# Kernel optimization log

Hardware: AMD Instinct MI355X
Metric: run time of the kernel (lower is better)

## Reference

```python
import jax, jax.numpy as jnp
import numpy as np

N_NODES = 100000
N_EDGES = 1600000
IN_DIM = 128
HID = 128
HEADS = 4
HEAD_DIM = HID // HEADS
OUT_DIM = 3
N_GRAPHS = 1024
BN_EPS = 1e-5


def setup_inputs() -> dict:
    key = jax.random.key(0)
    ks = jax.random.split(key, 32)
    inp = {}
    inp['x'] = jax.random.normal(ks[0], (N_NODES, IN_DIM), dtype=jnp.float32)
    inp['edge_index'] = jax.random.randint(ks[1], (2, N_EDGES), 0, N_NODES, dtype=jnp.int64)
    inp['edge_attr'] = jax.random.normal(ks[2], (N_EDGES,), dtype=jnp.float32)
    inp['batch'] = jnp.sort(jax.random.randint(ks[3], (N_NODES,), 0, N_GRAPHS, dtype=jnp.int64))
    s = 0.05
    inp['gat_w'] = jax.random.normal(ks[4], (IN_DIM, HID), jnp.float32) * s
    inp['gat_att_src'] = jax.random.normal(ks[5], (HEADS, HEAD_DIM), jnp.float32) * s
    inp['gat_att_dst'] = jax.random.normal(ks[6], (HEADS, HEAD_DIM), jnp.float32) * s
    inp['gat_b'] = jnp.zeros((HID,), jnp.float32)
    for i, k in zip((1, 2, 3), (ks[7], ks[8], ks[9])):
        inp[f'gcn{i}_w'] = jax.random.normal(k, (HID, HID), jnp.float32) * s
        inp[f'gcn{i}_b'] = jnp.zeros((HID,), jnp.float32)
        inp[f'bn{i}_g'] = jnp.ones((HID,), jnp.float32)
        inp[f'bn{i}_b'] = jnp.zeros((HID,), jnp.float32)
        inp[f'bn{i}_m'] = jax.random.normal(jax.random.fold_in(key, 100 + i), (HID,), jnp.float32) * 0.01
        inp[f'bn{i}_v'] = jnp.ones((HID,), jnp.float32)
    inp['p1_w'] = jax.random.normal(ks[10], (HID, HID), jnp.float32) * s
    inp['p1_b'] = jnp.zeros((HID,), jnp.float32)
    inp['p2_w'] = jax.random.normal(ks[11], (HID, HID // 2), jnp.float32) * s
    inp['p2_b'] = jnp.zeros((HID // 2,), jnp.float32)
    inp['cls_w'] = jax.random.normal(ks[12], (HID // 2, OUT_DIM), jnp.float32) * s
    inp['cls_b'] = jnp.zeros((OUT_DIM,), jnp.float32)
    return inp


def _add_self_loops(edge_index, n):
    ar = jnp.arange(n, dtype=edge_index.dtype)
    return jnp.concatenate([edge_index, jnp.stack([ar, ar])], axis=1)


def _gat(x, ei, w, att_src, att_dst, bias):
    # PyG GATConv: per-head linear, additive attention, softmax over incoming edges.
    n = x.shape[0]
    h = (x @ w).reshape(n, HEADS, HEAD_DIM)
    a_src = jnp.einsum('nhd,hd->nh', h, att_src)  # [N,H]
    a_dst = jnp.einsum('nhd,hd->nh', h, att_dst)
    src, dst = ei[0], ei[1]
    e = jax.nn.leaky_relu(a_src[src] + a_dst[dst], 0.2)  # [E,H]
    m = jax.ops.segment_max(e, dst, num_segments=n)       # per-dst max
    e = jnp.exp(e - m[dst])
    denom = jax.ops.segment_sum(e, dst, num_segments=n)
    alpha = e / denom[dst]                                 # self-loops => denom > 0
    msg = h[src] * alpha[:, :, None]                       # [E,H,D]
    out = jax.ops.segment_sum(msg, dst, num_segments=n)
    return out.reshape(n, HID) + bias


def _gcn(x, ei, w, bias):
    # PyG GCNConv with symmetric normalization and self-loops (already added).
    n = x.shape[0]
    src, dst = ei[0], ei[1]
    deg = jax.ops.segment_sum(jnp.ones_like(dst, dtype=x.dtype), dst, num_segments=n)
    dinv = jnp.where(deg > 0, jax.lax.rsqrt(deg), 0.0)
    norm = dinv[src] * dinv[dst]                           # [E]
    xw = x @ w
    out = jax.ops.segment_sum(norm[:, None] * xw[src], dst, num_segments=n)
    return out + bias


def _bn(x, g, b, m, v):
    return (x - m) * jax.lax.rsqrt(v + BN_EPS) * g + b


def reference(x, edge_index, edge_attr, batch,
              gat_w, gat_att_src, gat_att_dst, gat_b,
              gcn1_w, gcn1_b, gcn2_w, gcn2_b, gcn3_w, gcn3_b,
              bn1_g, bn1_b, bn1_m, bn1_v,
              bn2_g, bn2_b, bn2_m, bn2_v,
              bn3_g, bn3_b, bn3_m, bn3_v,
              p1_w, p1_b, p2_w, p2_b, cls_w, cls_b):
    n = x.shape[0]
    ei = _add_self_loops(edge_index, n)
    # eval mode: dropout is identity, BN uses running stats
    h = jax.nn.elu(_gat(x, ei, gat_w, gat_att_src, gat_att_dst, gat_b))
    idn = h
    h = jax.nn.elu(_bn(_gcn(h, ei, gcn1_w, gcn1_b), bn1_g, bn1_b, bn1_m, bn1_v)) + idn
    idn = h
    h = jax.nn.elu(_bn(_gcn(h, ei, gcn2_w, gcn2_b), bn2_g, bn2_b, bn2_m, bn2_v)) + idn
    h = jax.nn.elu(_bn(_gcn(h, ei, gcn3_w, gcn3_b), bn3_g, bn3_b, bn3_m, bn3_v))
    # global mean pool over graphs
    sums = jax.ops.segment_sum(h, batch, num_segments=N_GRAPHS)
    cnts = jax.ops.segment_sum(jnp.ones((n,), h.dtype), batch, num_segments=N_GRAPHS)
    g = sums / jnp.maximum(cnts, 1.0)[:, None]
    emb = jax.nn.elu(g @ p1_w + p1_b)
    emb = emb @ p2_w + p2_b
    out = emb @ cls_w + cls_b
    return out, emb
```

## Files before the change

### kernel.cpp

```cpp
#include <hip/hip_runtime.h>
#include <math.h>

#define BN_EPS 1e-5f
typedef unsigned short u16;
typedef __attribute__((ext_vector_type(8))) short bf16x8;
typedef __attribute__((ext_vector_type(4))) float f32x4;

__device__ inline unsigned bfpack2(float a, float b){
  unsigned ua = __float_as_uint(a); ua = (ua + 0x7fffu + ((ua >> 16) & 1u)) >> 16;
  unsigned ub = __float_as_uint(b); ub = (ub + 0x7fffu + ((ub >> 16) & 1u)) >> 16;
  return ua | (ub << 16);
}
__device__ inline u16 bf16of(float a){
  unsigned ua = __float_as_uint(a); return (u16)((ua + 0x7fffu + ((ua >> 16) & 1u)) >> 16);
}
__device__ inline float bflo(unsigned u){ return __uint_as_float(u << 16); }
__device__ inline float bfhi(unsigned u){ return __uint_as_float(u & 0xffff0000u); }

__global__ void k_count(const int* __restrict__ ei, int E, int N, int* __restrict__ deg){
  int chunk = blockIdx.x & 7;
  int e = (blockIdx.x >> 3)*256 + threadIdx.x;
  int ET = E + N;
  if (e >= ET) return;
  int csz = (N + 7) >> 3;
  int lo = chunk*csz, hi = lo + csz; if (hi > N) hi = N;
  int dst = (e < E) ? ei[E + e] : (e - E);
  if (dst < lo || dst >= hi) return;
  atomicAdd(&deg[dst], 1);
}

__global__ __launch_bounds__(1024) void k_scan_block(const int* __restrict__ deg, int* __restrict__ offs,
                                                     int* __restrict__ part, int N){
  __shared__ int sh[1024];
  int t = threadIdx.x; int i = blockIdx.x*1024 + t;
  int v = (i < N) ? deg[i] : 0;
  sh[t] = v; __syncthreads();
  for (int off = 1; off < 1024; off <<= 1){
    int u = (t >= off) ? sh[t - off] : 0;
    __syncthreads();
    sh[t] += u;
    __syncthreads();
  }
  if (i < N) offs[i] = sh[t] - v;
  if (t == 1023) part[blockIdx.x] = sh[1023];
}

__global__ void k_scan_part(int* part, int nb){
  if (threadIdx.x == 0 && blockIdx.x == 0){
    int s = 0;
    for (int i = 0; i < nb; ++i){ int v = part[i]; part[i] = s; s += v; }
  }
}

__global__ void k_add_part(int* __restrict__ offs, const int* __restrict__ part, int N){
  int i = blockIdx.x*256 + threadIdx.x;
  if (i < N) offs[i] += part[i >> 10];
}

__global__ void k_fill(const int* __restrict__ ei, int E, int N, const int* __restrict__ offs,
                       int* __restrict__ cursor, int* __restrict__ csr){
  int chunk = blockIdx.x & 7;
  int e = (blockIdx.x >> 3)*256 + threadIdx.x;
  int ET = E + N;
  if (e >= ET) return;
  int csz = (N + 7) >> 3;
  int lo = chunk*csz, hi = lo + csz; if (hi > N) hi = N;
  int src, dst;
  if (e < E){
    dst = ei[E + e];
    if (dst < lo || dst >= hi) return;
    src = ei[e];
  } else {
    src = e - E; dst = src;
    if (dst < lo || dst >= hi) return;
  }
  int pos = offs[dst] + atomicAdd(&cursor[dst], 1);
  csr[pos] = src;
}

__global__ void k_wconv(const float* __restrict__ W, u16* __restrict__ WbT){
  int id = blockIdx.x*256 + threadIdx.x;
  int nn = id >> 7, kk = id & 127;
  WbT[id] = bf16of(W[kk*128 + nn]);
}

__global__ __launch_bounds__(256, 2) void k_gemm_mfma(const float* __restrict__ A,
                                                      const u16* __restrict__ WbT,
                                                      u16* __restrict__ Yb, int M,
                                                      const int* __restrict__ deg){
  int lane = threadIdx.x & 63;
  int wv   = threadIdx.x >> 6;
  int row0 = blockIdx.x * 64 + wv * 16;
  int rA   = row0 + (lane & 15);
  if (rA >= M) rA = M - 1;
  int g    = lane >> 4;

  bf16x8 afr[4];
  const float* ap = A + (size_t)rA*128 + g*8;
  #pragma unroll
  for (int s = 0; s < 4; ++s){
    float4 f0 = *(const float4*)(ap + s*32);
    float4 f1 = *(const float4*)(ap + s*32 + 4);
    union { bf16x8 v; unsigned u[4]; } tmp;
    tmp.u[0] = bfpack2(f0.x, f0.y);
    tmp.u[1] = bfpack2(f0.z, f0.w);
    tmp.u[2] = bfpack2(f1.x, f1.y);
    tmp.u[3] = bfpack2(f1.z, f1.w);
    afr[s] = tmp.v;
  }

  f32x4 acc[8] = {};
  #pragma unroll
  for (int s = 0; s < 4; ++s){
    union BU { uint4 q; bf16x8 v; } b[8];
    #pragma unroll
    for (int t = 0; t < 8; ++t){
      int col = t*16 + (lane & 15);
      b[t].q = ((const uint4*)(WbT + (size_t)col*128))[s*4 + g];
    }
    #pragma unroll
    for (int t = 0; t < 8; ++t)
      acc[t] = __builtin_amdgcn_mfma_f32_16x16x32_bf16(afr[s], b[t].v, acc[t], 0, 0, 0);
  }

  int orow = row0 + (lane >> 4)*4;
  #pragma unroll
  for (int j = 0; j < 4; ++j){
    int r = orow + j;
    if (r < M){
      float sc = deg ? rsqrtf((float)deg[r]) : 1.0f;
      #pragma unroll
      for (int t = 0; t < 8; ++t)
        Yb[(size_t)r*128 + t*16 + (lane & 15)] = bf16of(acc[t][j] * sc);
    }
  }
}

__global__ __launch_bounds__(256) void k_attn(const unsigned* __restrict__ Yb, const float* __restrict__ asrcw,
                                              const float* __restrict__ adstw,
                                              float* __restrict__ a_src, float* __restrict__ a_dst, int N){
  int n = (blockIdx.x*256 + threadIdx.x) >> 6;
  int lane = threadIdx.x & 63;
  if (n >= N) return;
  int head = lane >> 4;
  int d0 = (lane & 15) * 2;
  unsigned u = Yb[(size_t)n*64 + lane];
  float h0 = bflo(u), h1 = bfhi(u);
  float vs = h0 * asrcw[head*32 + d0] + h1 * asrcw[head*32 + d0 + 1];
  float vd = h0 * adstw[head*32 + d0] + h1 * adstw[head*32 + d0 + 1];
  #pragma unroll
  for (int m = 1; m < 16; m <<= 1){
    vs += __shfl_xor(vs, m, 64);
    vd += __shfl_xor(vd, m, 64);
  }
  if ((lane & 15) == 0){
    a_src[n*4 + head] = vs;
    a_dst[n*4 + head] = vd;
  }
}

__global__ __launch_bounds__(256) void k_edge_w(const int* __restrict__ csr, const int* __restrict__ offs,
                                                const int* __restrict__ deg,
                                                const float4* __restrict__ asrc4, const float4* __restrict__ adst4,
                                                float4* __restrict__ wE, int N){
  int n = blockIdx.x*16 + (threadIdx.x >> 4);
  int l16 = threadIdx.x & 15;
  if (n >= N) return;
  int beg = offs[n], d = deg[n];
  float4 ad = adst4[n];
  for (int i = l16; i < d; i += 16){
    float4 as = asrc4[csr[beg + i]];
    float e0 = as.x + ad.x; e0 = e0 > 0.f ? e0 : 0.2f*e0;
    float e1 = as.y + ad.y; e1 = e1 > 0.f ? e1 : 0.2f*e1;
    float e2 = as.z + ad.z; e2 = e2 > 0.f ? e2 : 0.2f*e2;
    float e3 = as.w + ad.w; e3 = e3 > 0.f ? e3 : 0.2f*e3;
    wE[beg + i] = make_float4(__expf(e0), __expf(e1), __expf(e2), __expf(e3));
  }
}

__global__ __launch_bounds__(256) void k_gat_agg(const uint4* __restrict__ Yb4, const int* __restrict__ csr,
                                                 const int* __restrict__ offs, const int* __restrict__ deg,
                                                 const float* __restrict__ wE, const float* __restrict__ bias,
                                                 float* __restrict__ out, int N){
  int n = blockIdx.x*16 + (threadIdx.x >> 4);
  int l = threadIdx.x & 15;
  if (n >= N) return;
  int head = l >> 2;
  int beg = offs[n], d = deg[n];
  const int* cp = csr + beg;
  const float* wp = wE + (size_t)beg*4 + head;
  float a[8] = {};
  float sw = 0.f;
  for (int i = 0; i < d; i += 4){
    int j1 = (i+1 < d) ? i+1 : i;
    int j2 = (i+2 < d) ? i+2 : i;
    int j3 = (i+3 < d) ? i+3 : i;
    int n0 = cp[i], n1 = cp[j1], n2 = cp[j2], n3 = cp[j3];
    uint4 v0 = Yb4[(size_t)n0*16 + l];
    uint4 v1 = Yb4[(size_t)n1*16 + l];
    uint4 v2 = Yb4[(size_t)n2*16 + l];
    uint4 v3 = Yb4[(size_t)n3*16 + l];
    float w0 = wp[(size_t)i*4];
    float w1 = (i+1 < d) ? wp[(size_t)j1*4] : 0.f;
    float w2 = (i+2 < d) ? wp[(size_t)j2*4] : 0.f;
    float w3 = (i+3 < d) ? wp[(size_t)j3*4] : 0.f;
    sw += (w0 + w1) + (w2 + w3);
    unsigned u0[4] = {v0.x, v0.y, v0.z, v0.w};
    unsigned u1[4] = {v1.x, v1.y, v1.z, v1.w};
    unsigned u2[4] = {v2.x, v2.y, v2.z, v2.w};
    unsigned u3[4] = {v3.x, v3.y, v3.z, v3.w};
    #pragma unroll
    for (int c = 0; c < 4; ++c){
      a[2*c]   += w0*bflo(u0[c]) + w1*bflo(u1[c]) + w2*bflo(u2[c]) + w3*bflo(u3[c]);
      a[2*c+1] += w0*bfhi(u0[c]) + w1*bfhi(u1[c]) + w2*bfhi(u2[c]) + w3*bfhi(u3[c]);
    }
  }
  float inv = 1.f / sw;
  int c0 = l*8;
  float4 b0 = *(const float4*)(bias + c0);
  float4 b1 = *(const float4*)(bias + c0 + 4);
  float bb8[8] = {b0.x,b0.y,b0.z,b0.w,b1.x,b1.y,b1.z,b1.w};
  float og[8];
  #pragma unroll
  for (int c = 0; c < 8; ++c){
    float z = a[c]*inv + bb8[c];
    og[c] = z > 0.f ? z : expm1f(z);
  }
  float* op = out + (size_t)n*128 + c0;
  *(float4*)op       = make_float4(og[0],og[1],og[2],og[3]);
  *(float4*)(op + 4) = make_float4(og[4],og[5],og[6],og[7]);
}

__global__ __launch_bounds__(256) void k_gcn_agg(const uint4* __restrict__ Yb4, const float* __restrict__ resid,
                                                 float* __restrict__ out, const int* __restrict__ csr,
                                                 const int* __restrict__ offs, const int* __restrict__ deg,
                                                 const float* __restrict__ gb, const float* __restrict__ bg,
                                                 const float* __restrict__ bb, const float* __restrict__ bm,
                                                 const float* __restrict__ bv, int N){
  int n = blockIdx.x*16 + (threadIdx.x >> 4);
  int l = threadIdx.x & 15;
  if (n >= N) return;
  int beg = offs[n], d = deg[n];
  const int* cp = csr + beg;
  float a[8] = {};
  for (int i = 0; i < d; i += 4){
    int j1 = (i+1 < d) ? i+1 : i;
    int j2 = (i+2 < d) ? i+2 : i;
    int j3 = (i+3 < d) ? i+3 : i;
    int n0 = cp[i], n1 = cp[j1], n2 = cp[j2], n3 = cp[j3];
    uint4 v0 = Yb4[(size_t)n0*16 + l];
    uint4 v1 = Yb4[(size_t)n1*16 + l];
    uint4 v2 = Yb4[(size_t)n2*16 + l];
    uint4 v3 = Yb4[(size_t)n3*16 + l];
    float m1 = (i+1 < d) ? 1.f : 0.f;
    float m2 = (i+2 < d) ? 1.f : 0.f;
    float m3 = (i+3 < d) ? 1.f : 0.f;
    unsigned u0[4] = {v0.x, v0.y, v0.z, v0.w};
    unsigned u1[4] = {v1.x, v1.y, v1.z, v1.w};
    unsigned u2[4] = {v2.x, v2.y, v2.z, v2.w};
    unsigned u3[4] = {v3.x, v3.y, v3.z, v3.w};
    #pragma unroll
    for (int c = 0; c < 4; ++c){
      a[2*c]   += bflo(u0[c]) + m1*bflo(u1[c]) + m2*bflo(u2[c]) + m3*bflo(u3[c]);
      a[2*c+1] += bfhi(u0[c]) + m1*bfhi(u1[c]) + m2*bfhi(u2[c]) + m3*bfhi(u3[c]);
    }
  }
  float dinv = rsqrtf((float)d);
  int c0 = l*8;
  float4 g0  = *(const float4*)(bg + c0),  g1  = *(const float4*)(bg + c0 + 4);
  float4 bb0 = *(const float4*)(bb + c0),  bb1 = *(const float4*)(bb + c0 + 4);
  float4 m0  = *(const float4*)(bm + c0),  m1v = *(const float4*)(bm + c0 + 4);
  float4 v0  = *(const float4*)(bv + c0),  v1  = *(const float4*)(bv + c0 + 4);
  float4 q0  = *(const float4*)(gb + c0),  q1  = *(const float4*)(gb + c0 + 4);
  float gg[8]  = {g0.x,g0.y,g0.z,g0.w,g1.x,g1.y,g1.z,g1.w};
  float bbb[8] = {bb0.x,bb0.y,bb0.z,bb0.w,bb1.x,bb1.y,bb1.z,bb1.w};
  float mmm[8] = {m0.x,m0.y,m0.z,m0.w,m1v.x,m1v.y,m1v.z,m1v.w};
  float vvv[8] = {v0.x,v0.y,v0.z,v0.w,v1.x,v1.y,v1.z,v1.w};
  float qqq[8] = {q0.x,q0.y,q0.z,q0.w,q1.x,q1.y,q1.z,q1.w};
  float og[8];
  const float* rp = resid ? (resid + (size_t)n*128 + c0) : nullptr;
  float4 r0, r1;
  if (rp){ r0 = *(const float4*)rp; r1 = *(const float4*)(rp + 4); }
  float rr[8];
  if (rp){ rr[0]=r0.x; rr[1]=r0.y; rr[2]=r0.z; rr[3]=r0.w; rr[4]=r1.x; rr[5]=r1.y; rr[6]=r1.z; rr[7]=r1.w; }
  #pragma unroll
  for (int c = 0; c < 8; ++c){
    float As = gg[c] * rsqrtf(vvv[c] + BN_EPS);
    float z = a[c]*dinv*As + (qqq[c] - mmm[c])*As + bbb[c];
    z = z > 0.f ? z : expm1f(z);
    if (rp) z += rr[c];
    og[c] = z;
  }
  float* op = out + (size_t)n*128 + c0;
  *(float4*)op       = make_float4(og[0],og[1],og[2],og[3]);
  *(float4*)(op + 4) = make_float4(og[4],og[5],og[6],og[7]);
}

__global__ __launch_bounds__(128) void k_pool(const float* __restrict__ H, const int* __restrict__ batch,
                                              float* __restrict__ G, int N){
  int gid = blockIdx.x; int c = threadIdx.x;
  int lo = 0, hi = N;
  while (lo < hi){ int mid = (lo + hi) >> 1; if (batch[mid] < gid) lo = mid + 1; else hi = mid; }
  int start = lo;
  lo = start; hi = N;
  while (lo < hi){ int mid = (lo + hi) >> 1; if (batch[mid] < gid + 1) lo = mid + 1; else hi = mid; }
  int end = lo;
  float acc = 0.f;
  for (int r = start; r < end; ++r) acc += H[(size_t)r*128 + c];
  float cnt = (float)(end - start);
  G[gid*128 + c] = acc / fmaxf(cnt, 1.0f);
}

__global__ __launch_bounds__(128) void k_mlp(const float* __restrict__ G, const float* __restrict__ p1w,
                                             const float* __restrict__ p1b, const float* __restrict__ p2w,
                                             const float* __restrict__ p2b, const float* __restrict__ cw,
                                             const float* __restrict__ cb, float* __restrict__ out, int NG){
  int gid = blockIdx.x; int t = threadIdx.x;
  __shared__ float gv[128], t1[128], e[64];
  gv[t] = G[gid*128 + t];
  __syncthreads();
  float acc = p1b[t];
  for (int k = 0; k < 128; ++k) acc += gv[k] * p1w[k*128 + t];
  t1[t] = acc > 0.f ? acc : expm1f(acc);
  __syncthreads();
  if (t < 64){
    float a = p2b[t];
    for (int k = 0; k < 128; ++k) a += t1[k] * p2w[k*64 + t];
    e[t] = a;
    out[NG*3 + gid*64 + t] = a;
  }
  __syncthreads();
  if (t < 3){
    float a = cb[t];
    for (int k = 0; k < 64; ++k) a += e[k] * cw[k*3 + t];
    out[gid*3 + t] = a;
  }
}

extern "C" void kernel_launch(void* const* d_in, const int* in_sizes, int n_in,
                              void* d_out, int out_size, void* d_ws, size_t ws_size,
                              hipStream_t stream){
  const float* x      = (const float*)d_in[0];
  const int*   ei     = (const int*)d_in[1];
  const int*   batch  = (const int*)d_in[3];
  const float* gat_w  = (const float*)d_in[4];
  const float* att_s  = (const float*)d_in[5];
  const float* att_d  = (const float*)d_in[6];
  const float* gat_b  = (const float*)d_in[7];
  const float* w1 = (const float*)d_in[8];  const float* b1 = (const float*)d_in[9];
  const float* bn1g = (const float*)d_in[10], *bn1b = (const float*)d_in[11],
             * bn1m = (const float*)d_in[12], *bn1v = (const float*)d_in[13];
  const float* w2 = (const float*)d_in[14]; const float* b2 = (const float*)d_in[15];
  const float* bn2g = (const float*)d_in[16], *bn2b = (const float*)d_in[17],
             * bn2m = (const float*)d_in[18], *bn2v = (const float*)d_in[19];
  const float* w3 = (const float*)d_in[20]; const float* b3 = (const float*)d_in[21];
  const float* bn3g = (const float*)d_in[22], *bn3b = (const float*)d_in[23],
             * bn3m = (const float*)d_in[24], *bn3v = (const float*)d_in[25];
  const float* p1w = (const float*)d_in[26]; const float* p1b = (const float*)d_in[27];
  const float* p2w = (const float*)d_in[28]; const float* p2b = (const float*)d_in[29];
  const float* cw  = (const float*)d_in[30]; const float* cb  = (const float*)d_in[31];

  int N  = in_sizes[3];
  int E  = in_sizes[1] / 2;
  int ET = E + N;
  int NG = out_size / 67;

  char* ws = (char*)d_ws;
  size_t off = 0;
  auto alloc = [&](size_t bytes) -> void* {
    void* p = ws + off;
    off = (off + bytes + 255) & ~(size_t)255;
    return p;
  };
  float*    A    = (float*)alloc((size_t)N * 128 * 4);
  float*    Bact = (float*)alloc((size_t)N * 128 * 4);
  u16*      Yb   = (u16*)alloc((size_t)N * 128 * 2);
  int*      csr  = (int*)alloc((size_t)ET * 4);
  int*      deg  = (int*)alloc((size_t)N * 4);
  int*      offs = (int*)alloc((size_t)N * 4);
  int*      curs = (int*)alloc((size_t)N * 4);
  int*      part = (int*)alloc(1024 * 4);
  float*    asrc = (float*)alloc((size_t)N * 4 * 4);
  float*    adst = (float*)alloc((size_t)N * 4 * 4);
  float*    wE   = (float*)alloc((size_t)ET * 4 * 4);
  float*    G    = (float*)alloc((size_t)NG * 128 * 4);
  u16*      WbG  = (u16*)alloc(16384 * 2);
  u16*      Wb1  = (u16*)alloc(16384 * 2);
  u16*      Wb2  = (u16*)alloc(16384 * 2);
  u16*      Wb3  = (u16*)alloc(16384 * 2);

  hipMemsetAsync(deg,  0, (size_t)N * 4, stream);
  hipMemsetAsync(curs, 0, (size_t)N * 4, stream);

  int nb = (N + 1023) / 1024;
  int bpp = (ET + 255)/256;
  k_count<<<8*bpp, 256, 0, stream>>>(ei, E, N, deg);
  k_scan_block<<<nb, 1024, 0, stream>>>(deg, offs, part, N);
  k_scan_part<<<1, 1, 0, stream>>>(part, nb);
  k_add_part<<<(N + 255)/256, 256, 0, stream>>>(offs, part, N);
  k_fill<<<8*bpp, 256, 0, stream>>>(ei, E, N, offs, curs, csr);

  k_wconv<<<64, 256, 0, stream>>>(gat_w, WbG);
  k_wconv<<<64, 256, 0, stream>>>(w1, Wb1);
  k_wconv<<<64, 256, 0, stream>>>(w2, Wb2);
  k_wconv<<<64, 256, 0, stream>>>(w3, Wb3);

  int gblk = (N + 63) / 64;
  int nblk16 = (N + 15) / 16;
  int ablk = (N + 3) / 4;

  k_gemm_mfma<<<gblk, 256, 0, stream>>>(x, WbG, Yb, N, nullptr);
  k_attn<<<ablk, 256, 0, stream>>>((const unsigned*)Yb, att_s, att_d, asrc, adst, N);
  k_edge_w<<<nblk16, 256, 0, stream>>>(csr, offs, deg, (const float4*)asrc, (const float4*)adst,
                                       (float4*)wE, N);
  k_gat_agg<<<nblk16, 256, 0, stream>>>((const uint4*)Yb, csr, offs, deg, wE, gat_b, A, N);

  k_gemm_mfma<<<gblk, 256, 0, stream>>>(A, Wb1, Yb, N, deg);
  k_gcn_agg<<<nblk16, 256, 0, stream>>>((const uint4*)Yb, A, Bact, csr, offs, deg, b1, bn1g, bn1b, bn1m, bn1v, N);
  k_gemm_mfma<<<gblk, 256, 0, stream>>>(Bact, Wb2, Yb, N, deg);
  k_gcn_agg<<<nblk16, 256, 0, stream>>>((const uint4*)Yb, Bact, A, csr, offs, deg, b2, bn2g, bn2b, bn2m, bn2v, N);
  k_gemm_mfma<<<gblk, 256, 0, stream>>>(A, Wb3, Yb, N, deg);
  k_gcn_agg<<<nblk16, 256, 0, stream>>>((const uint4*)Yb, nullptr, Bact, csr, offs, deg, b3, bn3g, bn3b, bn3m, bn3v, N);

  k_pool<<<NG, 128, 0, stream>>>(Bact, batch, G, N);
  k_mlp<<<NG, 128, 0, stream>>>(G, p1w, p1b, p2w, p2b, cw, cb, (float*)d_out, NG);
}
```

Before: 666.6 us.

## Pad CSR rows to multiples of four, fuse edge weights into GAT aggregation

```diff
diff --git a/kernel.cpp b/kernel.cpp
--- a/kernel.cpp
+++ b/kernel.cpp
@@ -33,7 +33,7 @@
                                                      int* __restrict__ part, int N){
   __shared__ int sh[1024];
   int t = threadIdx.x; int i = blockIdx.x*1024 + t;
-  int v = (i < N) ? deg[i] : 0;
+  int v = (i < N) ? ((deg[i] + 3) & ~3) : 0;
   sh[t] = v; __syncthreads();
   for (int off = 1; off < 1024; off <<= 1){
     int u = (t >= off) ? sh[t - off] : 0;
@@ -52,9 +52,15 @@
   }
 }
 
-__global__ void k_add_part(int* __restrict__ offs, const int* __restrict__ part, int N){
+__global__ void k_add_part(int* __restrict__ offs, const int* __restrict__ part,
+                           const int* __restrict__ deg, int* __restrict__ csr, int N){
   int i = blockIdx.x*256 + threadIdx.x;
-  if (i < N) offs[i] += part[i >> 10];
+  if (i >= N) return;
+  int o = offs[i] + part[i >> 10];
+  offs[i] = o;
+  int d = deg[i];
+  int dp = (d + 3) & ~3;
+  for (int j = d; j < dp; ++j) csr[o + j] = N;
 }
 
 __global__ void k_fill(const int* __restrict__ ei, int E, int N, const int* __restrict__ offs,
@@ -84,6 +90,21 @@
   WbT[id] = bf16of(W[kk*128 + nn]);
 }
 
+__global__ void k_bnfold(const float* b1, const float* g1, const float* bb1, const float* m1, const float* v1,
+                         const float* b2, const float* g2, const float* bb2, const float* m2, const float* v2,
+                         const float* b3, const float* g3, const float* bb3, const float* m3, const float* v3,
+                         float* __restrict__ S, float* __restrict__ T){
+  int t = threadIdx.x;
+  int layer = t >> 7, c = t & 127;
+  const float *gb, *g, *bb, *m, *v;
+  if (layer == 0){ gb=b1; g=g1; bb=bb1; m=m1; v=v1; }
+  else if (layer == 1){ gb=b2; g=g2; bb=bb2; m=m2; v=v2; }
+  else { gb=b3; g=g3; bb=bb3; m=m3; v=v3; }
+  float s = g[c] * rsqrtf(v[c] + BN_EPS);
+  S[t] = s;
+  T[t] = (gb[c] - m[c]) * s + bb[c];
+}
+
 __global__ __launch_bounds__(256, 2) void k_gemm_mfma(const float* __restrict__ A,
                                                       const u16* __restrict__ WbT,
                                                       u16* __restrict__ Yb, int M,
@@ -139,6 +160,7 @@
 __global__ __launch_bounds__(256) void k_attn(const unsigned* __restrict__ Yb, const float* __restrict__ asrcw,
                                               const float* __restrict__ adstw,
                                               float* __restrict__ a_src, float* __restrict__ a_dst, int N){
+  if (blockIdx.x == 0 && threadIdx.x < 4) a_src[(size_t)N*4 + threadIdx.x] = -1e38f;
   int n = (blockIdx.x*256 + threadIdx.x) >> 6;
   int lane = threadIdx.x & 63;
   if (n >= N) return;
@@ -159,51 +181,36 @@
   }
 }
 
-__global__ __launch_bounds__(256) void k_edge_w(const int* __restrict__ csr, const int* __restrict__ offs,
-                                                const int* __restrict__ deg,
-                                                const float4* __restrict__ asrc4, const float4* __restrict__ adst4,
-                                                float4* __restrict__ wE, int N){
-  int n = blockIdx.x*16 + (threadIdx.x >> 4);
-  int l16 = threadIdx.x & 15;
-  if (n >= N) return;
-  int beg = offs[n], d = deg[n];
-  float4 ad = adst4[n];
-  for (int i = l16; i < d; i += 16){
-    float4 as = asrc4[csr[beg + i]];
-    float e0 = as.x + ad.x; e0 = e0 > 0.f ? e0 : 0.2f*e0;
-    float e1 = as.y + ad.y; e1 = e1 > 0.f ? e1 : 0.2f*e1;
-    float e2 = as.z + ad.z; e2 = e2 > 0.f ? e2 : 0.2f*e2;
-    float e3 = as.w + ad.w; e3 = e3 > 0.f ? e3 : 0.2f*e3;
-    wE[beg + i] = make_float4(__expf(e0), __expf(e1), __expf(e2), __expf(e3));
-  }
-}
-
 __global__ __launch_bounds__(256) void k_gat_agg(const uint4* __restrict__ Yb4, const int* __restrict__ csr,
                                                  const int* __restrict__ offs, const int* __restrict__ deg,
-                                                 const float* __restrict__ wE, const float* __restrict__ bias,
-                                                 float* __restrict__ out, int N){
+                                                 const float* __restrict__ asrc, const float* __restrict__ adst,
+                                                 const float* __restrict__ bias, float* __restrict__ out, int N){
   int n = blockIdx.x*16 + (threadIdx.x >> 4);
   int l = threadIdx.x & 15;
   if (n >= N) return;
   int head = l >> 2;
   int beg = offs[n], d = deg[n];
+  int dp = (d + 3) & ~3;
   const int* cp = csr + beg;
-  const float* wp = wE + (size_t)beg*4 + head;
+  float adh = adst[n*4 + head];
   float a[8] = {};
   float sw = 0.f;
-  for (int i = 0; i < d; i += 4){
-    int j1 = (i+1 < d) ? i+1 : i;
-    int j2 = (i+2 < d) ? i+2 : i;
-    int j3 = (i+3 < d) ? i+3 : i;
-    int n0 = cp[i], n1 = cp[j1], n2 = cp[j2], n3 = cp[j3];
-    uint4 v0 = Yb4[(size_t)n0*16 + l];
-    uint4 v1 = Yb4[(size_t)n1*16 + l];
-    uint4 v2 = Yb4[(size_t)n2*16 + l];
-    uint4 v3 = Yb4[(size_t)n3*16 + l];
-    float w0 = wp[(size_t)i*4];
-    float w1 = (i+1 < d) ? wp[(size_t)j1*4] : 0.f;
-    float w2 = (i+2 < d) ? wp[(size_t)j2*4] : 0.f;
-    float w3 = (i+3 < d) ? wp[(size_t)j3*4] : 0.f;
+  uint4 idx = *(const uint4*)cp;
+  for (int i = 0; i < dp; i += 4){
+    int i2 = (i + 8 <= dp) ? i + 4 : i;
+    uint4 nxt = *(const uint4*)(cp + i2);
+    float e0 = asrc[(size_t)idx.x*4 + head] + adh;
+    float e1 = asrc[(size_t)idx.y*4 + head] + adh;
+    float e2 = asrc[(size_t)idx.z*4 + head] + adh;
+    float e3 = asrc[(size_t)idx.w*4 + head] + adh;
+    uint4 v0 = Yb4[(size_t)idx.x*16 + l];
+    uint4 v1 = Yb4[(size_t)idx.y*16 + l];
+    uint4 v2 = Yb4[(size_t)idx.z*16 + l];
+    uint4 v3 = Yb4[(size_t)idx.w*16 + l];
+    e0 = e0 > 0.f ? e0 : 0.2f*e0; float w0 = __expf(e0);
+    e1 = e1 > 0.f ? e1 : 0.2f*e1; float w1 = __expf(e1);
+    e2 = e2 > 0.f ? e2 : 0.2f*e2; float w2 = __expf(e2);
+    e3 = e3 > 0.f ? e3 : 0.2f*e3; float w3 = __expf(e3);
     sw += (w0 + w1) + (w2 + w3);
     unsigned u0[4] = {v0.x, v0.y, v0.z, v0.w};
     unsigned u1[4] = {v1.x, v1.y, v1.z, v1.w};
@@ -214,6 +221,7 @@
       a[2*c]   += w0*bflo(u0[c]) + w1*bflo(u1[c]) + w2*bflo(u2[c]) + w3*bflo(u3[c]);
       a[2*c+1] += w0*bfhi(u0[c]) + w1*bfhi(u1[c]) + w2*bfhi(u2[c]) + w3*bfhi(u3[c]);
     }
+    idx = nxt;
   }
   float inv = 1.f / sw;
   int c0 = l*8;
@@ -234,62 +242,51 @@
 __global__ __launch_bounds__(256) void k_gcn_agg(const uint4* __restrict__ Yb4, const float* __restrict__ resid,
                                                  float* __restrict__ out, const int* __restrict__ csr,
                                                  const int* __restrict__ offs, const int* __restrict__ deg,
-                                                 const float* __restrict__ gb, const float* __restrict__ bg,
-                                                 const float* __restrict__ bb, const float* __restrict__ bm,
-                                                 const float* __restrict__ bv, int N){
+                                                 const float* __restrict__ S, const float* __restrict__ T, int N){
   int n = blockIdx.x*16 + (threadIdx.x >> 4);
   int l = threadIdx.x & 15;
   if (n >= N) return;
   int beg = offs[n], d = deg[n];
+  int dp = (d + 3) & ~3;
   const int* cp = csr + beg;
   float a[8] = {};
-  for (int i = 0; i < d; i += 4){
-    int j1 = (i+1 < d) ? i+1 : i;
-    int j2 = (i+2 < d) ? i+2 : i;
-    int j3 = (i+3 < d) ? i+3 : i;
-    int n0 = cp[i], n1 = cp[j1], n2 = cp[j2], n3 = cp[j3];
-    uint4 v0 = Yb4[(size_t)n0*16 + l];
-    uint4 v1 = Yb4[(size_t)n1*16 + l];
-    uint4 v2 = Yb4[(size_t)n2*16 + l];
-    uint4 v3 = Yb4[(size_t)n3*16 + l];
-    float m1 = (i+1 < d) ? 1.f : 0.f;
-    float m2 = (i+2 < d) ? 1.f : 0.f;
-    float m3 = (i+3 < d) ? 1.f : 0.f;
+  uint4 idx = *(const uint4*)cp;
+  for (int i = 0; i < dp; i += 4){
+    int i2 = (i + 8 <= dp) ? i + 4 : i;
+    uint4 nxt = *(const uint4*)(cp + i2);
+    uint4 v0 = Yb4[(size_t)idx.x*16 + l];
+    uint4 v1 = Yb4[(size_t)idx.y*16 + l];
+    uint4 v2 = Yb4[(size_t)idx.z*16 + l];
+    uint4 v3 = Yb4[(size_t)idx.w*16 + l];
     unsigned u0[4] = {v0.x, v0.y, v0.z, v0.w};
     unsigned u1[4] = {v1.x, v1.y, v1.z, v1.w};
     unsigned u2[4] = {v2.x, v2.y, v2.z, v2.w};
     unsigned u3[4] = {v3.x, v3.y, v3.z, v3.w};
     #pragma unroll
     for (int c = 0; c < 4; ++c){
-      a[2*c]   += bflo(u0[c]) + m1*bflo(u1[c]) + m2*bflo(u2[c]) + m3*bflo(u3[c]);
-      a[2*c+1] += bfhi(u0[c]) + m1*bfhi(u1[c]) + m2*bfhi(u2[c]) + m3*bfhi(u3[c]);
+      a[2*c]   += (bflo(u0[c]) + bflo(u1[c])) + (bflo(u2[c]) + bflo(u3[c]));
+      a[2*c+1] += (bfhi(u0[c]) + bfhi(u1[c])) + (bfhi(u2[c]) + bfhi(u3[c]));
     }
+    idx = nxt;
   }
   float dinv = rsqrtf((float)d);
   int c0 = l*8;
-  float4 g0  = *(const float4*)(bg + c0),  g1  = *(const float4*)(bg + c0 + 4);
-  float4 bb0 = *(const float4*)(bb + c0),  bb1 = *(const float4*)(bb + c0 + 4);
-  float4 m0  = *(const float4*)(bm + c0),  m1v = *(const float4*)(bm + c0 + 4);
-  float4 v0  = *(const float4*)(bv + c0),  v1  = *(const float4*)(bv + c0 + 4);
-  float4 q0  = *(const float4*)(gb + c0),  q1  = *(const float4*)(gb + c0 + 4);
-  float gg[8]  = {g0.x,g0.y,g0.z,g0.w,g1.x,g1.y,g1.z,g1.w};
-  float bbb[8] = {bb0.x,bb0.y,bb0.z,bb0.w,bb1.x,bb1.y,bb1.z,bb1.w};
-  float mmm[8] = {m0.x,m0.y,m0.z,m0.w,m1v.x,m1v.y,m1v.z,m1v.w};
-  float vvv[8] = {v0.x,v0.y,v0.z,v0.w,v1.x,v1.y,v1.z,v1.w};
-  float qqq[8] = {q0.x,q0.y,q0.z,q0.w,q1.x,q1.y,q1.z,q1.w};
+  float4 S0 = *(const float4*)(S + c0), S1 = *(const float4*)(S + c0 + 4);
+  float4 T0 = *(const float4*)(T + c0), T1 = *(const float4*)(T + c0 + 4);
+  float ss[8] = {S0.x,S0.y,S0.z,S0.w,S1.x,S1.y,S1.z,S1.w};
+  float tt[8] = {T0.x,T0.y,T0.z,T0.w,T1.x,T1.y,T1.z,T1.w};
+  float rr[8] = {};
+  if (resid){
+    const float* rp = resid + (size_t)n*128 + c0;
+    float4 r0 = *(const float4*)rp, r1 = *(const float4*)(rp + 4);
+    rr[0]=r0.x; rr[1]=r0.y; rr[2]=r0.z; rr[3]=r0.w; rr[4]=r1.x; rr[5]=r1.y; rr[6]=r1.z; rr[7]=r1.w;
+  }
   float og[8];
-  const float* rp = resid ? (resid + (size_t)n*128 + c0) : nullptr;
-  float4 r0, r1;
-  if (rp){ r0 = *(const float4*)rp; r1 = *(const float4*)(rp + 4); }
-  float rr[8];
-  if (rp){ rr[0]=r0.x; rr[1]=r0.y; rr[2]=r0.z; rr[3]=r0.w; rr[4]=r1.x; rr[5]=r1.y; rr[6]=r1.z; rr[7]=r1.w; }
   #pragma unroll
   for (int c = 0; c < 8; ++c){
-    float As = gg[c] * rsqrtf(vvv[c] + BN_EPS);
-    float z = a[c]*dinv*As + (qqq[c] - mmm[c])*As + bbb[c];
+    float z = a[c]*dinv*ss[c] + tt[c];
     z = z > 0.f ? z : expm1f(z);
-    if (rp) z += rr[c];
-    og[c] = z;
+    og[c] = z + rr[c];
   }
   float* op = out + (size_t)n*128 + c0;
   *(float4*)op       = make_float4(og[0],og[1],og[2],og[3]);
@@ -374,36 +371,41 @@
   };
   float*    A    = (float*)alloc((size_t)N * 128 * 4);
   float*    Bact = (float*)alloc((size_t)N * 128 * 4);
-  u16*      Yb   = (u16*)alloc((size_t)N * 128 * 2);
-  int*      csr  = (int*)alloc((size_t)ET * 4);
+  u16*      Yb   = (u16*)alloc((size_t)(N + 1) * 128 * 2);
+  int*      csr  = (int*)alloc((size_t)(ET + 3*N) * 4);
   int*      deg  = (int*)alloc((size_t)N * 4);
   int*      offs = (int*)alloc((size_t)N * 4);
   int*      curs = (int*)alloc((size_t)N * 4);
   int*      part = (int*)alloc(1024 * 4);
-  float*    asrc = (float*)alloc((size_t)N * 4 * 4);
+  float*    asrc = (float*)alloc((size_t)(N + 1) * 4 * 4);
   float*    adst = (float*)alloc((size_t)N * 4 * 4);
-  float*    wE   = (float*)alloc((size_t)ET * 4 * 4);
   float*    G    = (float*)alloc((size_t)NG * 128 * 4);
   u16*      WbG  = (u16*)alloc(16384 * 2);
   u16*      Wb1  = (u16*)alloc(16384 * 2);
   u16*      Wb2  = (u16*)alloc(16384 * 2);
   u16*      Wb3  = (u16*)alloc(16384 * 2);
+  float*    bnS  = (float*)alloc(384 * 4);
+  float*    bnT  = (float*)alloc(384 * 4);
 
   hipMemsetAsync(deg,  0, (size_t)N * 4, stream);
   hipMemsetAsync(curs, 0, (size_t)N * 4, stream);
+  hipMemsetAsync(Yb + (size_t)N*128, 0, 256, stream);
 
   int nb = (N + 1023) / 1024;
   int bpp = (ET + 255)/256;
   k_count<<<8*bpp, 256, 0, stream>>>(ei, E, N, deg);
   k_scan_block<<<nb, 1024, 0, stream>>>(deg, offs, part, N);
   k_scan_part<<<1, 1, 0, stream>>>(part, nb);
-  k_add_part<<<(N + 255)/256, 256, 0, stream>>>(offs, part, N);
+  k_add_part<<<(N + 255)/256, 256, 0, stream>>>(offs, part, deg, csr, N);
   k_fill<<<8*bpp, 256, 0, stream>>>(ei, E, N, offs, curs, csr);
 
   k_wconv<<<64, 256, 0, stream>>>(gat_w, WbG);
   k_wconv<<<64, 256, 0, stream>>>(w1, Wb1);
   k_wconv<<<64, 256, 0, stream>>>(w2, Wb2);
   k_wconv<<<64, 256, 0, stream>>>(w3, Wb3);
+  k_bnfold<<<1, 384, 0, stream>>>(b1, bn1g, bn1b, bn1m, bn1v,
+                                  b2, bn2g, bn2b, bn2m, bn2v,
+                                  b3, bn3g, bn3b, bn3m, bn3v, bnS, bnT);
 
   int gblk = (N + 63) / 64;
   int nblk16 = (N + 15) / 16;
@@ -411,16 +413,14 @@
 
   k_gemm_mfma<<<gblk, 256, 0, stream>>>(x, WbG, Yb, N, nullptr);
   k_attn<<<ablk, 256, 0, stream>>>((const unsigned*)Yb, att_s, att_d, asrc, adst, N);
-  k_edge_w<<<nblk16, 256, 0, stream>>>(csr, offs, deg, (const float4*)asrc, (const float4*)adst,
-                                       (float4*)wE, N);
-  k_gat_agg<<<nblk16, 256, 0, stream>>>((const uint4*)Yb, csr, offs, deg, wE, gat_b, A, N);
+  k_gat_agg<<<nblk16, 256, 0, stream>>>((const uint4*)Yb, csr, offs, deg, asrc, adst, gat_b, A, N);
 
   k_gemm_mfma<<<gblk, 256, 0, stream>>>(A, Wb1, Yb, N, deg);
-  k_gcn_agg<<<nblk16, 256, 0, stream>>>((const uint4*)Yb, A, Bact, csr, offs, deg, b1, bn1g, bn1b, bn1m, bn1v, N);
+  k_gcn_agg<<<nblk16, 256, 0, stream>>>((const uint4*)Yb, A, Bact, csr, offs, deg, bnS, bnT, N);
   k_gemm_mfma<<<gblk, 256, 0, stream>>>(Bact, Wb2, Yb, N, deg);
-  k_gcn_agg<<<nblk16, 256, 0, stream>>>((const uint4*)Yb, Bact, A, csr, offs, deg, b2, bn2g, bn2b, bn2m, bn2v, N);
+  k_gcn_agg<<<nblk16, 256, 0, stream>>>((const uint4*)Yb, Bact, A, csr, offs, deg, bnS + 128, bnT + 128, N);
   k_gemm_mfma<<<gblk, 256, 0, stream>>>(A, Wb3, Yb, N, deg);
-  k_gcn_agg<<<nblk16, 256, 0, stream>>>((const uint4*)Yb, nullptr, Bact, csr, offs, deg, b3, bn3g, bn3b, bn3m, bn3v, N);
+  k_gcn_agg<<<nblk16, 256, 0, stream>>>((const uint4*)Yb, nullptr, Bact, csr, offs, deg, bnS + 256, bnT + 256, N);
 
   k_pool<<<NG, 128, 0, stream>>>(Bact, batch, G, N);
   k_mlp<<<NG, 128, 0, stream>>>(G, p1w, p1b, p2w, p2b, cw, cb, (float*)d_out, NG);
```

Measured after the change: 673.4 us. About the same (+1.0%).
